# Performance work log

Measured on AMD Instinct MI355X. Metric: run time of the kernel, lower is better.

## Reference

```python
import jax, jax.numpy as jnp
import numpy as np

A, B, S, AD, H, NH = 8, 32768, 128, 16, 64, 4
D = H // NH  # attend_dim = 16
MAX_ACTION = 1.0


def setup_inputs() -> dict:
    key = jax.random.key(0)
    ks = jax.random.split(key, 16)
    sc = 0.05
    return {
        'states': jax.random.normal(ks[0], (A, B, S), jnp.float32),
        'actions': jax.random.normal(ks[1], (A, B, AD), jnp.float32),
        'Ws': jax.random.normal(ks[2], (S, H), jnp.float32) * sc,
        'bs': jnp.zeros((H,), jnp.float32),
        'We': jax.random.normal(ks[3], (S + AD, H), jnp.float32) * sc,
        'be': jnp.zeros((H,), jnp.float32),
        'Wk': jax.random.normal(ks[4], (NH, H, D), jnp.float32) * sc,
        'Wsel': jax.random.normal(ks[5], (NH, H, D), jnp.float32) * sc,
        'Wv': jax.random.normal(ks[6], (NH, H, D), jnp.float32) * sc,
        'bv': jnp.zeros((NH, D), jnp.float32),
        'W1': jax.random.normal(ks[7], (2 * H, H), jnp.float32) * sc,
        'b1': jnp.zeros((H,), jnp.float32),
        'W2': jax.random.normal(ks[8], (H, 1), jnp.float32) * sc,
        'b2': jnp.zeros((1,), jnp.float32),
    }


def reference(states, actions, Ws, bs, We, be, Wk, Wsel, Wv, bv, W1, b1, W2, b2):
    # per-agent encoders (shared params, as in the torch module)
    s_enc = jax.nn.relu(jnp.einsum('abs,sh->abh', states, Ws) + bs)          # [A,B,H]
    sa = jnp.concatenate([states, actions / MAX_ACTION], axis=-1)            # [A,B,S+AD]
    sa_enc = jax.nn.relu(jnp.einsum('abi,ih->abh', sa, We) + be)             # [A,B,H]

    # per-head keys / values / selectors (n = head axis)
    keys = jnp.einsum('abh,nhd->nabd', sa_enc, Wk)                           # [NH,A,B,D]
    vals = jax.nn.relu(jnp.einsum('abh,nhd->nabd', sa_enc, Wv) + bv[:, None, None, :])
    sel = jnp.einsum('abh,nhd->nabd', s_enc, Wsel)                           # [NH,A,B,D]

    # exclude-self attention over agents == masked softmax over agent axis j
    logits = jnp.einsum('nibd,njbd->nibj', sel, keys) / jnp.sqrt(jnp.float32(D))
    self_mask = jnp.eye(A, dtype=bool)                                       # [A(i),A(j)]
    logits = jnp.where(self_mask[None, :, None, :], -1e9, logits)
    w = jax.nn.softmax(logits, axis=-1)                                      # [NH,A,B,A]
    other = jnp.einsum('nibj,njbd->nibd', w, vals)                           # [NH,A,B,D]
    other_cat = jnp.transpose(other, (1, 2, 0, 3)).reshape(A, B, NH * D)     # [A,B,H]

    critic_in = jnp.concatenate([sa_enc, other_cat], axis=-1)                # [A,B,2H]
    h = jax.nn.relu(jnp.einsum('abi,ih->abh', critic_in, W1) + b1)
    q = jnp.einsum('abh,ho->abo', h, W2) + b2                                # [A,B,1]
    return q
```

## Files before the change

kernel.cpp:

```cpp
#include <hip/hip_runtime.h>
#include <hip/hip_bf16.h>

#define A_N 8
#define B_N 32768
#define S_N 128
#define AD_N 16

typedef __attribute__((ext_vector_type(8))) short short8;
typedef __attribute__((ext_vector_type(4))) float floatx4;
typedef __attribute__((ext_vector_type(4))) int intx4;

#define MFMA16(a, b, c) __builtin_amdgcn_mfma_f32_16x16x32_bf16(a, b, c, 0, 0, 0)
#define SBAR() __builtin_amdgcn_sched_barrier(0)

__device__ __forceinline__ short f2bf(float f) {
    __hip_bfloat16 h = __float2bfloat16(f);
    return *reinterpret_cast<short*>(&h);
}
__device__ __forceinline__ int pk(float a, float b) {
    __hip_bfloat162 p = __float22bfloat162_rn(make_float2(a, b));
    return *reinterpret_cast<int*>(&p);
}
__device__ __forceinline__ short8 mk8(int a, int b, int c, int d) {
    intx4 v = {a, b, c, d};
    return *reinterpret_cast<short8*>(&v);
}
__device__ __forceinline__ void pk2(short8& r, int i, float a, float b) {
    __hip_bfloat162 p = __float22bfloat162_rn(make_float2(a, b));
    short2 s = *reinterpret_cast<short2*>(&p);
    r[i] = s.x; r[i + 1] = s.y;
}
__device__ __forceinline__ short8 cvt8(float4 x0, float4 x1) {
    short8 r;
    pk2(r, 0, x0.x, x0.y); pk2(r, 2, x0.z, x0.w);
    pk2(r, 4, x1.x, x1.y); pk2(r, 6, x1.z, x1.w);
    return r;
}

__device__ __forceinline__ int chperm(int p) {
    return 32 * (p >> 5) + 16 * ((p & 7) >> 2) + 4 * ((p >> 3) & 3) + (p & 3);
}

#define OFF_Ws   10240
#define OFF_Wk   18432
#define OFF_Wsel 22528
#define OFF_Wv   26624
#define OFF_W1   30720
#define W_TOTAL  38912

__global__ void prep_weights(const float* __restrict__ Ws, const float* __restrict__ We,
                             const float* __restrict__ be,
                             const float* __restrict__ Wk, const float* __restrict__ Wsel,
                             const float* __restrict__ Wv, const float* __restrict__ W1,
                             short* __restrict__ w) {
    int idx = blockIdx.x * 256 + threadIdx.x;
    if (idx >= W_TOTAL) return;
    float v = 0.f;
    int i, base;
    if (idx < OFF_Ws)        { i = idx;            base = 0; }
    else if (idx < OFF_Wk)   { i = idx - OFF_Ws;   base = 1; }
    else if (idx < OFF_Wsel) { i = idx - OFF_Wk;   base = 2; }
    else if (idx < OFF_Wv)   { i = idx - OFF_Wsel; base = 3; }
    else if (idx < OFF_W1)   { i = idx - OFF_Wv;   base = 4; }
    else                     { i = idx - OFF_W1;   base = 5; }
    const int e   = i & 7;
    const int f   = i >> 3;
    const int ch  = f & 63;
    const int slq = f >> 6;
    const int p   = (slq >> 2) * 32 + (slq & 3) * 8 + e;
    if (base == 0)      v = (p < 144) ? We[p * 64 + ch] : (p == 144 ? be[ch] : 0.f);
    else if (base == 1) v = Ws[p * 64 + ch];
    else if (base == 2) v = Wk[(ch >> 4) * 1024 + chperm(p) * 16 + (ch & 15)];
    else if (base == 3) v = Wsel[(ch >> 4) * 1024 + chperm(p) * 16 + (ch & 15)];
    else if (base == 4) v = Wv[(ch >> 4) * 1024 + chperm(p) * 16 + (ch & 15)];
    else                v = W1[chperm(p) * 64 + ch];
    w[idx] = f2bf(v);
}

#define TILES 4

__global__ __launch_bounds__(512, 4)
void attention_critic_mfma(
    const float* __restrict__ states, const float* __restrict__ actions,
    const float* __restrict__ bs, const float* __restrict__ bv,
    const float* __restrict__ b1, const float* __restrict__ W2,
    const float* __restrict__ b2,
    const short* __restrict__ wts, float* __restrict__ out)
{
    __shared__ __align__(16) short smem[W_TOTAL];

    const int tid  = threadIdx.x;
    const int wv   = tid >> 6;
    const int lane = tid & 63;
    const int lq   = lane >> 4;
    const int ln   = lane & 15;

    for (int c = wv; c < 76; c += 8) {
        const unsigned int* g = reinterpret_cast<const unsigned int*>(wts + c * 512) + lane * 4;
        __builtin_amdgcn_global_load_lds(g, reinterpret_cast<unsigned int*>(smem + c * 512), 16, 0, 0);
    }

    const int lo = lq * 512 + ln * 8;
    const short* lbA = smem + lo;
    const short* lbB = smem + OFF_Wv + lo;

    float bS4[4], bv4[4], b14[4], w24[4];
    #pragma unroll
    for (int nt = 0; nt < 4; ++nt) {
        bS4[nt] = bs[nt * 16 + ln];
        bv4[nt] = bv[nt * 16 + ln];
        b14[nt] = b1[nt * 16 + ln];
        w24[nt] = W2[nt * 16 + ln];
    }
    const float b2v = b2[0];

    const int bbase = blockIdx.x * (TILES * 16);
    const int aA  = ln & 7;
    const int blA = ln >> 3;
    const float* srow = states  + ((long)aA * B_N + bbase + wv * 2 + blA) * S_N;
    const float* arow = actions + ((long)aA * B_N + bbase + wv * 2 + blA) * AD_N;

    __syncthreads();

    const floatx4 z = {0.f, 0.f, 0.f, 0.f};

    #pragma unroll 1
    for (int t = 0; t < TILES; ++t) {
        const int b0 = bbase + t * 16;

        short8 xf[5];
        #pragma unroll
        for (int s = 0; s < 4; ++s) {
            float4 f0 = *reinterpret_cast<const float4*>(srow + s * 32 + lq * 8);
            float4 f1 = *reinterpret_cast<const float4*>(srow + s * 32 + lq * 8 + 4);
            xf[s] = cvt8(f0, f1);
        }
        {
            short8 xt = {0, 0, 0, 0, 0, 0, 0, 0};
            if (lq < 2) {
                float4 f0 = *reinterpret_cast<const float4*>(arow + lq * 8);
                float4 f1 = *reinterpret_cast<const float4*>(arow + lq * 8 + 4);
                xt = cvt8(f0, f1);
            } else if (lq == 2) {
                xt[0] = (short)0x3F80;
            }
            xf[4] = xt;
        }
        srow += 16 * S_N; arow += 16 * AD_N;

        short8 fE[2];
        {
            floatx4 accE[4] = {z, z, z, z};
            #pragma unroll
            for (int s = 0; s < 5; ++s)
                #pragma unroll
                for (int nt = 0; nt < 4; ++nt)
                    accE[nt] = MFMA16(*reinterpret_cast<const short8*>(lbA + s * 2048 + nt * 128), xf[s], accE[nt]);
            int pE[4][2];
            #pragma unroll
            for (int nt = 0; nt < 4; ++nt) {
                pE[nt][0] = pk(fmaxf(accE[nt][0], 0.f), fmaxf(accE[nt][1], 0.f));
                pE[nt][1] = pk(fmaxf(accE[nt][2], 0.f), fmaxf(accE[nt][3], 0.f));
            }
            fE[0] = mk8(pE[0][0], pE[0][1], pE[1][0], pE[1][1]);
            fE[1] = mk8(pE[2][0], pE[2][1], pE[3][0], pE[3][1]);
        }
        SBAR();

        short8 fS[2];
        {
            floatx4 accS[4] = {z, z, z, z};
            #pragma unroll
            for (int s = 0; s < 4; ++s)
                #pragma unroll
                for (int nt = 0; nt < 4; ++nt)
                    accS[nt] = MFMA16(*reinterpret_cast<const short8*>(lbA + OFF_Ws + s * 2048 + nt * 128), xf[s], accS[nt]);
            int pS[4][2];
            #pragma unroll
            for (int nt = 0; nt < 4; ++nt) {
                pS[nt][0] = pk(fmaxf(accS[nt][0] + bS4[nt], 0.f), fmaxf(accS[nt][1] + bS4[nt], 0.f));
                pS[nt][1] = pk(fmaxf(accS[nt][2] + bS4[nt], 0.f), fmaxf(accS[nt][3] + bS4[nt], 0.f));
            }
            fS[0] = mk8(pS[0][0], pS[0][1], pS[1][0], pS[1][1]);
            fS[1] = mk8(pS[2][0], pS[2][1], pS[3][0], pS[3][1]);
        }
        SBAR();

        int kp[4][2], sp[4][2];
        {
            floatx4 accK[4] = {z, z, z, z}, accSl[4] = {z, z, z, z};
            #pragma unroll
            for (int s = 0; s < 2; ++s)
                #pragma unroll
                for (int nt = 0; nt < 4; ++nt) {
                    accK[nt]  = MFMA16(*reinterpret_cast<const short8*>(lbA + OFF_Wk   + s * 2048 + nt * 128), fE[s], accK[nt]);
                    accSl[nt] = MFMA16(*reinterpret_cast<const short8*>(lbA + OFF_Wsel + s * 2048 + nt * 128), fS[s], accSl[nt]);
                }
            #pragma unroll
            for (int nt = 0; nt < 4; ++nt) {
                kp[nt][0] = pk(accK[nt][0],  accK[nt][1]);
                kp[nt][1] = pk(accK[nt][2],  accK[nt][3]);
                sp[nt][0] = pk(accSl[nt][0], accSl[nt][1]);
                sp[nt][1] = pk(accSl[nt][2], accSl[nt][3]);
            }
        }
        SBAR();

        int pV[4][2];
        {
            floatx4 accV[4] = {z, z, z, z};
            #pragma unroll
            for (int s = 0; s < 2; ++s)
                #pragma unroll
                for (int nt = 0; nt < 4; ++nt)
                    accV[nt] = MFMA16(fE[s], *reinterpret_cast<const short8*>(lbB + s * 2048 + nt * 128), accV[nt]);
            #pragma unroll
            for (int nt = 0; nt < 4; ++nt) {
                pV[nt][0] = pk(fmaxf(accV[nt][0] + bv4[nt], 0.f), fmaxf(accV[nt][1] + bv4[nt], 0.f));
                pV[nt][1] = pk(fmaxf(accV[nt][2] + bv4[nt], 0.f), fmaxf(accV[nt][3] + bv4[nt], 0.f));
            }
        }
        SBAR();

        int pO[4][2];
        {
            const bool sameb = ((lq >> 1) == (ln >> 3));
            #pragma unroll
            for (int nt = 0; nt < 4; ++nt) {
                short8 fa = mk8(kp[nt][0], kp[nt][1], 0, 0);
                short8 fb = mk8(sp[nt][0], sp[nt][1], 0, 0);
                floatx4 L = MFMA16(fa, fb, z);
                float lg[4];
                #pragma unroll
                for (int i = 0; i < 4; ++i) {
                    const bool valid = sameb && (4 * lq + i != ln);
                    lg[i] = valid ? L[i] * 0.25f : -1e9f;
                }
                float m = fmaxf(fmaxf(lg[0], lg[1]), fmaxf(lg[2], lg[3]));
                m = fmaxf(m, __shfl_xor(m, 16, 64));
                m = fmaxf(m, __shfl_xor(m, 32, 64));
                float e0 = __expf(lg[0] - m), e1 = __expf(lg[1] - m);
                float e2 = __expf(lg[2] - m), e3 = __expf(lg[3] - m);
                float ss = e0 + e1 + e2 + e3;
                ss += __shfl_xor(ss, 16, 64);
                ss += __shfl_xor(ss, 32, 64);
                const float inv = 1.f / ss;
                short8 fp = mk8(pk(e0 * inv, e1 * inv), pk(e2 * inv, e3 * inv), 0, 0);
                short8 fv = mk8(pV[nt][0], pV[nt][1], 0, 0);
                floatx4 O = MFMA16(fv, fp, z);
                pO[nt][0] = pk(O[0], O[1]);
                pO[nt][1] = pk(O[2], O[3]);
            }
        }
        SBAR();

        {
            short8 fO[2] = { mk8(pO[0][0], pO[0][1], pO[1][0], pO[1][1]),
                             mk8(pO[2][0], pO[2][1], pO[3][0], pO[3][1]) };
            floatx4 accH[4] = {z, z, z, z};
            #pragma unroll
            for (int s = 0; s < 4; ++s) {
                const short8 af = (s < 2) ? fE[s] : fO[s - 2];
                #pragma unroll
                for (int nt = 0; nt < 4; ++nt)
                    accH[nt] = MFMA16(af, *reinterpret_cast<const short8*>(lbB + 4096 + s * 2048 + nt * 128), accH[nt]);
            }
            float p0 = 0.f, p1 = 0.f, p2 = 0.f, p3 = 0.f;
            #pragma unroll
            for (int nt = 0; nt < 4; ++nt) {
                p0 += fmaxf(accH[nt][0] + b14[nt], 0.f) * w24[nt];
                p1 += fmaxf(accH[nt][1] + b14[nt], 0.f) * w24[nt];
                p2 += fmaxf(accH[nt][2] + b14[nt], 0.f) * w24[nt];
                p3 += fmaxf(accH[nt][3] + b14[nt], 0.f) * w24[nt];
            }
            #pragma unroll
            for (int mk = 1; mk < 16; mk <<= 1) {
                p0 += __shfl_xor(p0, mk, 64);
                p1 += __shfl_xor(p1, mk, 64);
                p2 += __shfl_xor(p2, mk, 64);
                p3 += __shfl_xor(p3, mk, 64);
            }
            if (ln == 0) {
                float pr[4] = {p0, p1, p2, p3};
                #pragma unroll
                for (int i = 0; i < 4; ++i) {
                    const int slot = lq * 4 + i;
                    out[(long)(slot & 7) * B_N + b0 + wv * 2 + (slot >> 3)] = pr[i] + b2v;
                }
            }
        }
        SBAR();
    }
}

extern "C" void kernel_launch(void* const* d_in, const int* in_sizes, int n_in,
                              void* d_out, int out_size, void* d_ws, size_t ws_size,
                              hipStream_t stream) {
    const float* states  = (const float*)d_in[0];
    const float* actions = (const float*)d_in[1];
    const float* Ws      = (const float*)d_in[2];
    const float* bs      = (const float*)d_in[3];
    const float* We      = (const float*)d_in[4];
    const float* be      = (const float*)d_in[5];
    const float* Wk      = (const float*)d_in[6];
    const float* Wsel    = (const float*)d_in[7];
    const float* Wv      = (const float*)d_in[8];
    const float* bv      = (const float*)d_in[9];
    const float* W1      = (const float*)d_in[10];
    const float* b1      = (const float*)d_in[11];
    const float* W2      = (const float*)d_in[12];
    const float* b2      = (const float*)d_in[13];
    short* wts = (short*)d_ws;
    float* out = (float*)d_out;

    prep_weights<<<(W_TOTAL + 255) / 256, 256, 0, stream>>>(Ws, We, be, Wk, Wsel, Wv, W1, wts);
    attention_critic_mfma<<<B_N / (TILES * 16), 512, 0, stream>>>(
        states, actions, bs, bv, b1, W2, b2, wts, out);
}
```

Measured before the change: 234.3 us.

## Process two batch tiles per iteration to reuse LDS weight fragments

Each loop iteration now handles two 16-column batch tiles at once. Every weight fragment read from LDS feeds two independent MFMA chains, which halves LDS weight traffic per tile and gives the scheduler more independent MFMAs. Blocks cover 128 batch columns, so half as many blocks launch. Launch bounds drop from 4 to 2 blocks per SM to allow the larger register footprint, which lowers occupancy and latency hiding for the global loads.

```diff
diff --git a/kernel.cpp b/kernel.cpp
--- a/kernel.cpp
+++ b/kernel.cpp
@@ -77,9 +77,9 @@
     w[idx] = f2bf(v);
 }
 
-#define TILES 4
-
-__global__ __launch_bounds__(512, 4)
+#define PAIRS 4
+
+__global__ __launch_bounds__(512, 2)
 void attention_critic_mfma(
     const float* __restrict__ states, const float* __restrict__ actions,
     const float* __restrict__ bs, const float* __restrict__ bv,
@@ -114,7 +114,7 @@
     }
     const float b2v = b2[0];
 
-    const int bbase = blockIdx.x * (TILES * 16);
+    const int bbase = blockIdx.x * (PAIRS * 32);
     const int aA  = ln & 7;
     const int blA = ln >> 3;
     const float* srow = states  + ((long)aA * B_N + bbase + wv * 2 + blA) * S_N;
@@ -125,167 +125,216 @@
     const floatx4 z = {0.f, 0.f, 0.f, 0.f};
 
     #pragma unroll 1
-    for (int t = 0; t < TILES; ++t) {
-        const int b0 = bbase + t * 16;
-
-        short8 xf[5];
+    for (int t = 0; t < PAIRS; ++t) {
+        const int b0 = bbase + t * 32;
+
+        short8 xf0[5], xf1[5];
         #pragma unroll
         for (int s = 0; s < 4; ++s) {
-            float4 f0 = *reinterpret_cast<const float4*>(srow + s * 32 + lq * 8);
-            float4 f1 = *reinterpret_cast<const float4*>(srow + s * 32 + lq * 8 + 4);
-            xf[s] = cvt8(f0, f1);
-        }
-        {
-            short8 xt = {0, 0, 0, 0, 0, 0, 0, 0};
+            float4 a0 = *reinterpret_cast<const float4*>(srow + s * 32 + lq * 8);
+            float4 a1 = *reinterpret_cast<const float4*>(srow + s * 32 + lq * 8 + 4);
+            float4 c0 = *reinterpret_cast<const float4*>(srow + 16 * S_N + s * 32 + lq * 8);
+            float4 c1 = *reinterpret_cast<const float4*>(srow + 16 * S_N + s * 32 + lq * 8 + 4);
+            xf0[s] = cvt8(a0, a1);
+            xf1[s] = cvt8(c0, c1);
+        }
+        {
+            short8 t0 = {0, 0, 0, 0, 0, 0, 0, 0}, t1 = t0;
             if (lq < 2) {
-                float4 f0 = *reinterpret_cast<const float4*>(arow + lq * 8);
-                float4 f1 = *reinterpret_cast<const float4*>(arow + lq * 8 + 4);
-                xt = cvt8(f0, f1);
+                float4 a0 = *reinterpret_cast<const float4*>(arow + lq * 8);
+                float4 a1 = *reinterpret_cast<const float4*>(arow + lq * 8 + 4);
+                float4 c0 = *reinterpret_cast<const float4*>(arow + 16 * AD_N + lq * 8);
+                float4 c1 = *reinterpret_cast<const float4*>(arow + 16 * AD_N + lq * 8 + 4);
+                t0 = cvt8(a0, a1);
+                t1 = cvt8(c0, c1);
             } else if (lq == 2) {
-                xt[0] = (short)0x3F80;
-            }
-            xf[4] = xt;
-        }
-        srow += 16 * S_N; arow += 16 * AD_N;
-
-        short8 fE[2];
-        {
-            floatx4 accE[4] = {z, z, z, z};
+                t0[0] = (short)0x3F80;
+                t1[0] = (short)0x3F80;
+            }
+            xf0[4] = t0; xf1[4] = t1;
+        }
+        srow += 32 * S_N; arow += 32 * AD_N;
+
+        short8 fE0[2], fE1[2];
+        {
+            floatx4 acc0[4] = {z, z, z, z}, acc1[4] = {z, z, z, z};
             #pragma unroll
             for (int s = 0; s < 5; ++s)
                 #pragma unroll
-                for (int nt = 0; nt < 4; ++nt)
-                    accE[nt] = MFMA16(*reinterpret_cast<const short8*>(lbA + s * 2048 + nt * 128), xf[s], accE[nt]);
-            int pE[4][2];
+                for (int nt = 0; nt < 4; ++nt) {
+                    short8 wf = *reinterpret_cast<const short8*>(lbA + s * 2048 + nt * 128);
+                    acc0[nt] = MFMA16(wf, xf0[s], acc0[nt]);
+                    acc1[nt] = MFMA16(wf, xf1[s], acc1[nt]);
+                }
+            int p0[4][2], p1[4][2];
             #pragma unroll
             for (int nt = 0; nt < 4; ++nt) {
-                pE[nt][0] = pk(fmaxf(accE[nt][0], 0.f), fmaxf(accE[nt][1], 0.f));
-                pE[nt][1] = pk(fmaxf(accE[nt][2], 0.f), fmaxf(accE[nt][3], 0.f));
-            }
-            fE[0] = mk8(pE[0][0], pE[0][1], pE[1][0], pE[1][1]);
-            fE[1] = mk8(pE[2][0], pE[2][1], pE[3][0], pE[3][1]);
-        }
-        SBAR();
-
-        short8 fS[2];
-        {
-            floatx4 accS[4] = {z, z, z, z};
+                p0[nt][0] = pk(fmaxf(acc0[nt][0], 0.f), fmaxf(acc0[nt][1], 0.f));
+                p0[nt][1] = pk(fmaxf(acc0[nt][2], 0.f), fmaxf(acc0[nt][3], 0.f));
+                p1[nt][0] = pk(fmaxf(acc1[nt][0], 0.f), fmaxf(acc1[nt][1], 0.f));
+                p1[nt][1] = pk(fmaxf(acc1[nt][2], 0.f), fmaxf(acc1[nt][3], 0.f));
+            }
+            fE0[0] = mk8(p0[0][0], p0[0][1], p0[1][0], p0[1][1]);
+            fE0[1] = mk8(p0[2][0], p0[2][1], p0[3][0], p0[3][1]);
+            fE1[0] = mk8(p1[0][0], p1[0][1], p1[1][0], p1[1][1]);
+            fE1[1] = mk8(p1[2][0], p1[2][1], p1[3][0], p1[3][1]);
+        }
+        SBAR();
+
+        short8 fS0[2], fS1[2];
+        {
+            floatx4 acc0[4] = {z, z, z, z}, acc1[4] = {z, z, z, z};
             #pragma unroll
             for (int s = 0; s < 4; ++s)
                 #pragma unroll
-                for (int nt = 0; nt < 4; ++nt)
-                    accS[nt] = MFMA16(*reinterpret_cast<const short8*>(lbA + OFF_Ws + s * 2048 + nt * 128), xf[s], accS[nt]);
-            int pS[4][2];
+                for (int nt = 0; nt < 4; ++nt) {
+                    short8 wf = *reinterpret_cast<const short8*>(lbA + OFF_Ws + s * 2048 + nt * 128);
+                    acc0[nt] = MFMA16(wf, xf0[s], acc0[nt]);
+                    acc1[nt] = MFMA16(wf, xf1[s], acc1[nt]);
+                }
+            int p0[4][2], p1[4][2];
             #pragma unroll
             for (int nt = 0; nt < 4; ++nt) {
-                pS[nt][0] = pk(fmaxf(accS[nt][0] + bS4[nt], 0.f), fmaxf(accS[nt][1] + bS4[nt], 0.f));
-                pS[nt][1] = pk(fmaxf(accS[nt][2] + bS4[nt], 0.f), fmaxf(accS[nt][3] + bS4[nt], 0.f));
-            }
-            fS[0] = mk8(pS[0][0], pS[0][1], pS[1][0], pS[1][1]);
-            fS[1] = mk8(pS[2][0], pS[2][1], pS[3][0], pS[3][1]);
-        }
-        SBAR();
-
-        int kp[4][2], sp[4][2];
-        {
-            floatx4 accK[4] = {z, z, z, z}, accSl[4] = {z, z, z, z};
+                p0[nt][0] = pk(fmaxf(acc0[nt][0] + bS4[nt], 0.f), fmaxf(acc0[nt][1] + bS4[nt], 0.f));
+                p0[nt][1] = pk(fmaxf(acc0[nt][2] + bS4[nt], 0.f), fmaxf(acc0[nt][3] + bS4[nt], 0.f));
+                p1[nt][0] = pk(fmaxf(acc1[nt][0] + bS4[nt], 0.f), fmaxf(acc1[nt][1] + bS4[nt], 0.f));
+                p1[nt][1] = pk(fmaxf(acc1[nt][2] + bS4[nt], 0.f), fmaxf(acc1[nt][3] + bS4[nt], 0.f));
+            }
+            fS0[0] = mk8(p0[0][0], p0[0][1], p0[1][0], p0[1][1]);
+            fS0[1] = mk8(p0[2][0], p0[2][1], p0[3][0], p0[3][1]);
+            fS1[0] = mk8(p1[0][0], p1[0][1], p1[1][0], p1[1][1]);
+            fS1[1] = mk8(p1[2][0], p1[2][1], p1[3][0], p1[3][1]);
+        }
+        SBAR();
+
+        int kp0[4][2], sp0[4][2], kp1[4][2], sp1[4][2];
+        {
+            floatx4 aK0[4] = {z, z, z, z}, aS0[4] = {z, z, z, z};
+            floatx4 aK1[4] = {z, z, z, z}, aS1[4] = {z, z, z, z};
             #pragma unroll
             for (int s = 0; s < 2; ++s)
                 #pragma unroll
                 for (int nt = 0; nt < 4; ++nt) {
-                    accK[nt]  = MFMA16(*reinterpret_cast<const short8*>(lbA + OFF_Wk   + s * 2048 + nt * 128), fE[s], accK[nt]);
-                    accSl[nt] = MFMA16(*reinterpret_cast<const short8*>(lbA + OFF_Wsel + s * 2048 + nt * 128), fS[s], accSl[nt]);
+                    short8 wk = *reinterpret_cast<const short8*>(lbA + OFF_Wk   + s * 2048 + nt * 128);
+                    short8 ws = *reinterpret_cast<const short8*>(lbA + OFF_Wsel + s * 2048 + nt * 128);
+                    aK0[nt] = MFMA16(wk, fE0[s], aK0[nt]);
+                    aK1[nt] = MFMA16(wk, fE1[s], aK1[nt]);
+                    aS0[nt] = MFMA16(ws, fS0[s], aS0[nt]);
+                    aS1[nt] = MFMA16(ws, fS1[s], aS1[nt]);
                 }
             #pragma unroll
             for (int nt = 0; nt < 4; ++nt) {
-                kp[nt][0] = pk(accK[nt][0],  accK[nt][1]);
-                kp[nt][1] = pk(accK[nt][2],  accK[nt][3]);
-                sp[nt][0] = pk(accSl[nt][0], accSl[nt][1]);
-                sp[nt][1] = pk(accSl[nt][2], accSl[nt][3]);
-            }
-        }
-        SBAR();
-
-        int pV[4][2];
-        {
-            floatx4 accV[4] = {z, z, z, z};
+                kp0[nt][0] = pk(aK0[nt][0], aK0[nt][1]); kp0[nt][1] = pk(aK0[nt][2], aK0[nt][3]);
+                sp0[nt][0] = pk(aS0[nt][0], aS0[nt][1]); sp0[nt][1] = pk(aS0[nt][2], aS0[nt][3]);
+                kp1[nt][0] = pk(aK1[nt][0], aK1[nt][1]); kp1[nt][1] = pk(aK1[nt][2], aK1[nt][3]);
+                sp1[nt][0] = pk(aS1[nt][0], aS1[nt][1]); sp1[nt][1] = pk(aS1[nt][2], aS1[nt][3]);
+            }
+        }
+        SBAR();
+
+        int pV0[4][2], pV1[4][2];
+        {
+            floatx4 a0[4] = {z, z, z, z}, a1[4] = {z, z, z, z};
             #pragma unroll
             for (int s = 0; s < 2; ++s)
                 #pragma unroll
-                for (int nt = 0; nt < 4; ++nt)
-                    accV[nt] = MFMA16(fE[s], *reinterpret_cast<const short8*>(lbB + s * 2048 + nt * 128), accV[nt]);
+                for (int nt = 0; nt < 4; ++nt) {
+                    short8 wf = *reinterpret_cast<const short8*>(lbB + s * 2048 + nt * 128);
+                    a0[nt] = MFMA16(fE0[s], wf, a0[nt]);
+                    a1[nt] = MFMA16(fE1[s], wf, a1[nt]);
+                }
             #pragma unroll
             for (int nt = 0; nt < 4; ++nt) {
-                pV[nt][0] = pk(fmaxf(accV[nt][0] + bv4[nt], 0.f), fmaxf(accV[nt][1] + bv4[nt], 0.f));
-                pV[nt][1] = pk(fmaxf(accV[nt][2] + bv4[nt], 0.f), fmaxf(accV[nt][3] + bv4[nt], 0.f));
-            }
-        }
-        SBAR();
-
-        int pO[4][2];
+                pV0[nt][0] = pk(fmaxf(a0[nt][0] + bv4[nt], 0.f), fmaxf(a0[nt][1] + bv4[nt], 0.f));
+                pV0[nt][1] = pk(fmaxf(a0[nt][2] + bv4[nt], 0.f), fmaxf(a0[nt][3] + bv4[nt], 0.f));
+                pV1[nt][0] = pk(fmaxf(a1[nt][0] + bv4[nt], 0.f), fmaxf(a1[nt][1] + bv4[nt], 0.f));
+                pV1[nt][1] = pk(fmaxf(a1[nt][2] + bv4[nt], 0.f), fmaxf(a1[nt][3] + bv4[nt], 0.f));
+            }
+        }
+        SBAR();
+
+        int pO0[4][2], pO1[4][2];
         {
             const bool sameb = ((lq >> 1) == (ln >> 3));
             #pragma unroll
-            for (int nt = 0; nt < 4; ++nt) {
-                short8 fa = mk8(kp[nt][0], kp[nt][1], 0, 0);
-                short8 fb = mk8(sp[nt][0], sp[nt][1], 0, 0);
-                floatx4 L = MFMA16(fa, fb, z);
-                float lg[4];
-                #pragma unroll
-                for (int i = 0; i < 4; ++i) {
-                    const bool valid = sameb && (4 * lq + i != ln);
-                    lg[i] = valid ? L[i] * 0.25f : -1e9f;
-                }
-                float m = fmaxf(fmaxf(lg[0], lg[1]), fmaxf(lg[2], lg[3]));
-                m = fmaxf(m, __shfl_xor(m, 16, 64));
-                m = fmaxf(m, __shfl_xor(m, 32, 64));
-                float e0 = __expf(lg[0] - m), e1 = __expf(lg[1] - m);
-                float e2 = __expf(lg[2] - m), e3 = __expf(lg[3] - m);
-                float ss = e0 + e1 + e2 + e3;
-                ss += __shfl_xor(ss, 16, 64);
-                ss += __shfl_xor(ss, 32, 64);
-                const float inv = 1.f / ss;
-                short8 fp = mk8(pk(e0 * inv, e1 * inv), pk(e2 * inv, e3 * inv), 0, 0);
-                short8 fv = mk8(pV[nt][0], pV[nt][1], 0, 0);
-                floatx4 O = MFMA16(fv, fp, z);
-                pO[nt][0] = pk(O[0], O[1]);
-                pO[nt][1] = pk(O[2], O[3]);
-            }
-        }
-        SBAR();
-
-        {
-            short8 fO[2] = { mk8(pO[0][0], pO[0][1], pO[1][0], pO[1][1]),
-                             mk8(pO[2][0], pO[2][1], pO[3][0], pO[3][1]) };
-            floatx4 accH[4] = {z, z, z, z};
+            for (int tt = 0; tt < 2; ++tt) {
+                int (*kp)[2] = tt ? kp1 : kp0;
+                int (*sp)[2] = tt ? sp1 : sp0;
+                int (*pV)[2] = tt ? pV1 : pV0;
+                int (*pO)[2] = tt ? pO1 : pO0;
+                #pragma unroll
+                for (int nt = 0; nt < 4; ++nt) {
+                    short8 fa = mk8(kp[nt][0], kp[nt][1], 0, 0);
+                    short8 fb = mk8(sp[nt][0], sp[nt][1], 0, 0);
+                    floatx4 L = MFMA16(fa, fb, z);
+                    float lg[4];
+                    #pragma unroll
+                    for (int i = 0; i < 4; ++i) {
+                        const bool valid = sameb && (4 * lq + i != ln);
+                        lg[i] = valid ? L[i] * 0.25f : -1e9f;
+                    }
+                    float m = fmaxf(fmaxf(lg[0], lg[1]), fmaxf(lg[2], lg[3]));
+                    m = fmaxf(m, __shfl_xor(m, 16, 64));
+                    m = fmaxf(m, __shfl_xor(m, 32, 64));
+                    float e0 = __expf(lg[0] - m), e1 = __expf(lg[1] - m);
+                    float e2 = __expf(lg[2] - m), e3 = __expf(lg[3] - m);
+                    float ss = e0 + e1 + e2 + e3;
+                    ss += __shfl_xor(ss, 16, 64);
+                    ss += __shfl_xor(ss, 32, 64);
+                    const float inv = 1.f / ss;
+                    short8 fp = mk8(pk(e0 * inv, e1 * inv), pk(e2 * inv, e3 * inv), 0, 0);
+                    short8 fv = mk8(pV[nt][0], pV[nt][1], 0, 0);
+                    floatx4 O = MFMA16(fv, fp, z);
+                    pO[nt][0] = pk(O[0], O[1]);
+                    pO[nt][1] = pk(O[2], O[3]);
+                }
+            }
+        }
+        SBAR();
+
+        {
+            short8 fO0[2] = { mk8(pO0[0][0], pO0[0][1], pO0[1][0], pO0[1][1]),
+                              mk8(pO0[2][0], pO0[2][1], pO0[3][0], pO0[3][1]) };
+            short8 fO1[2] = { mk8(pO1[0][0], pO1[0][1], pO1[1][0], pO1[1][1]),
+                              mk8(pO1[2][0], pO1[2][1], pO1[3][0], pO1[3][1]) };
+            floatx4 aH0[4] = {z, z, z, z}, aH1[4] = {z, z, z, z};
             #pragma unroll
             for (int s = 0; s < 4; ++s) {
-                const short8 af = (s < 2) ? fE[s] : fO[s - 2];
-                #pragma unroll
-                for (int nt = 0; nt < 4; ++nt)
-                    accH[nt] = MFMA16(af, *reinterpret_cast<const short8*>(lbB + 4096 + s * 2048 + nt * 128), accH[nt]);
-            }
-            float p0 = 0.f, p1 = 0.f, p2 = 0.f, p3 = 0.f;
-            #pragma unroll
-            for (int nt = 0; nt < 4; ++nt) {
-                p0 += fmaxf(accH[nt][0] + b14[nt], 0.f) * w24[nt];
-                p1 += fmaxf(accH[nt][1] + b14[nt], 0.f) * w24[nt];
-                p2 += fmaxf(accH[nt][2] + b14[nt], 0.f) * w24[nt];
-                p3 += fmaxf(accH[nt][3] + b14[nt], 0.f) * w24[nt];
-            }
-            #pragma unroll
-            for (int mk = 1; mk < 16; mk <<= 1) {
-                p0 += __shfl_xor(p0, mk, 64);
-                p1 += __shfl_xor(p1, mk, 64);
-                p2 += __shfl_xor(p2, mk, 64);
-                p3 += __shfl_xor(p3, mk, 64);
-            }
-            if (ln == 0) {
-                float pr[4] = {p0, p1, p2, p3};
-                #pragma unroll
-                for (int i = 0; i < 4; ++i) {
-                    const int slot = lq * 4 + i;
-                    out[(long)(slot & 7) * B_N + b0 + wv * 2 + (slot >> 3)] = pr[i] + b2v;
+                const short8 a0 = (s < 2) ? fE0[s] : fO0[s - 2];
+                const short8 a1 = (s < 2) ? fE1[s] : fO1[s - 2];
+                #pragma unroll
+                for (int nt = 0; nt < 4; ++nt) {
+                    short8 w1 = *reinterpret_cast<const short8*>(lbB + 4096 + s * 2048 + nt * 128);
+                    aH0[nt] = MFMA16(a0, w1, aH0[nt]);
+                    aH1[nt] = MFMA16(a1, w1, aH1[nt]);
+                }
+            }
+            #pragma unroll
+            for (int tt = 0; tt < 2; ++tt) {
+                floatx4* aH = tt ? aH1 : aH0;
+                float p0 = 0.f, p1 = 0.f, p2 = 0.f, p3 = 0.f;
+                #pragma unroll
+                for (int nt = 0; nt < 4; ++nt) {
+                    p0 += fmaxf(aH[nt][0] + b14[nt], 0.f) * w24[nt];
+                    p1 += fmaxf(aH[nt][1] + b14[nt], 0.f) * w24[nt];
+                    p2 += fmaxf(aH[nt][2] + b14[nt], 0.f) * w24[nt];
+                    p3 += fmaxf(aH[nt][3] + b14[nt], 0.f) * w24[nt];
+                }
+                #pragma unroll
+                for (int mk = 1; mk < 16; mk <<= 1) {
+                    p0 += __shfl_xor(p0, mk, 64);
+                    p1 += __shfl_xor(p1, mk, 64);
+                    p2 += __shfl_xor(p2, mk, 64);
+                    p3 += __shfl_xor(p3, mk, 64);
+                }
+                if (ln == 0) {
+                    float pr[4] = {p0, p1, p2, p3};
+                    const int bt = b0 + tt * 16;
+                    #pragma unroll
+                    for (int i = 0; i < 4; ++i) {
+                        const int slot = lq * 4 + i;
+                        out[(long)(slot & 7) * B_N + bt + wv * 2 + (slot >> 3)] = pr[i] + b2v;
+                    }
                 }
             }
         }
@@ -314,6 +363,6 @@
     float* out = (float*)d_out;
 
     prep_weights<<<(W_TOTAL + 255) / 256, 256, 0, stream>>>(Ws, We, be, Wk, Wsel, Wv, W1, wts);
-    attention_critic_mfma<<<B_N / (TILES * 16), 512, 0, stream>>>(
+    attention_critic_mfma<<<B_N / (PAIRS * 32), 512, 0, stream>>>(
         states, actions, bs, bv, b1, W2, b2, wts, out);
 }
```

Result: no change. 234.9 us (+0.2%).
